# Kernel tuning notes

Hardware: AMD Instinct MI355X
Metric: run time of the kernel (lower is better)

## Reference

```python
import jax, jax.numpy as jnp
import numpy as np

N_PAIRS = 300_000
N_CENTERS = 10_000
N_SPECIES = 4
N_PSEUDO = 4
N_RADIAL = 20
L_MAX = 3


def setup_inputs() -> dict:
    key = jax.random.key(0)
    ks = jax.random.split(key, 8)
    inp = {}
    for l in range(L_MAX + 1):
        inp[f"vec_l{l}"] = jax.random.normal(ks[l], (N_PAIRS, 2 * l + 1, N_RADIAL), dtype=jnp.float32)
    # combination_matrix: Linear(n_species -> n_pseudo, bias=False) => weight [n_pseudo, n_species]
    inp["W"] = jax.random.normal(ks[4], (N_PSEUDO, N_SPECIES), dtype=jnp.float32) / np.sqrt(N_SPECIES)
    inp["species_neighbor"] = jax.random.randint(ks[5], (N_PAIRS,), 0, N_SPECIES, dtype=jnp.int64)
    inp["density_indices"] = jax.random.randint(ks[6], (N_PAIRS,), 0, N_CENTERS, dtype=jnp.int64)
    inp["n_centers"] = N_CENTERS
    return inp


def reference(vec_l0, vec_l1, vec_l2, vec_l3, W, species_neighbor, density_indices, n_centers):
    # one-hot species of neighbor, then Linear (no bias): weights [P, n_pseudo]
    one_hot_aj = jax.nn.one_hot(species_neighbor, W.shape[1], dtype=W.dtype)
    pseudo_w = one_hot_aj @ W.T  # [P, n_pseudo]
    outs = []
    for vec in (vec_l0, vec_l1, vec_l2, vec_l3):
        # outer product: [P, 2l+1, n_radial, n_pseudo]
        src = jnp.einsum('pcn,pd->pcnd', vec, pseudo_w)
        # scatter-add over unique (structure, center) groups
        dens = jax.ops.segment_sum(src, density_indices, num_segments=n_centers)
        nc, comp, nl, npse = dens.shape
        # [n_centers, 2l+1, n_pseudo, n_radial] -> flatten (pseudo-major features)
        dens = dens.swapaxes(2, 3).reshape(nc, comp * npse * nl)
        outs.append(dens)
    # concatenate all l-channels for a single output array
    return jnp.concatenate(outs, axis=1)
```

## Files before the change

### kernel.cpp

```cpp
#include <hip/hip_runtime.h>

#define N_PAIRS   300000
#define N_CENTERS 10000
#define N_FEAT    1280
#define PF        4


__global__ void hist_k(const int* __restrict__ didx, int* __restrict__ counts) {
    int p = blockIdx.x * blockDim.x + threadIdx.x;
    if (p < N_PAIRS) atomicAdd(&counts[didx[p]], 1);
}

__global__ void scan_k(const int* __restrict__ counts,
                       int* __restrict__ offsets, int* __restrict__ cursor) {
    __shared__ int part[1024];
    int t = threadIdx.x;
    const int CH = 10;
    int base = t * CH;
    int loc[CH];
    int s = 0;
    #pragma unroll
    for (int j = 0; j < CH; ++j) {
        int v = (base + j < N_CENTERS) ? counts[base + j] : 0;
        loc[j] = s; s += v;
    }
    part[t] = s;
    __syncthreads();
    for (int off = 1; off < 1024; off <<= 1) {
        int v   = part[t];
        int add = (t >= off) ? part[t - off] : 0;
        __syncthreads();
        part[t] = v + add;
        __syncthreads();
    }
    int prefix = (t > 0) ? part[t - 1] : 0;
    #pragma unroll
    for (int j = 0; j < CH; ++j) {
        int idx = base + j;
        if (idx < N_CENTERS) {
            int o = prefix + loc[j];
            offsets[idx] = o;
            cursor[idx]  = o;
        }
    }
    if (t == 1023) offsets[N_CENTERS] = part[1023];
}

__global__ void scatter_k(const int* __restrict__ didx,
                          int* __restrict__ cursor, int* __restrict__ pair_ids) {
    int p = blockIdx.x * blockDim.x + threadIdx.x;
    if (p < N_PAIRS) {
        int c = didx[p];
        int pos = atomicAdd(&cursor[c], 1);
        pair_ids[pos] = p;
    }
}


__global__ __launch_bounds__(320) void accum_k(
    const float* __restrict__ vec0, const float* __restrict__ vec1,
    const float* __restrict__ vec2, const float* __restrict__ vec3,
    const float* __restrict__ W,    const int* __restrict__ species,
    const int* __restrict__ offsets, const int* __restrict__ pair_ids,
    float* __restrict__ out) {
    __shared__ float  ldsW[16];
    __shared__ float  ldsWp[PF * 4];
    __shared__ float4 ldsv[PF * 80];

    const int t = threadIdx.x;
    const int c = blockIdx.x;
    if (t < 16) ldsW[t] = W[t];

    const int q = t / 80;
    const int u = t - q * 80;

    const float* src; int rowlen, foff;
    if (u < 5)       { src = vec0; rowlen = 20;  foff = u;      }
    else if (u < 20) { src = vec1; rowlen = 60;  foff = u - 5;  }
    else if (u < 45) { src = vec2; rowlen = 100; foff = u - 20; }
    else             { src = vec3; rowlen = 140; foff = u - 45; }

    const int g0 = 4 * u;
    int fb, vb;
    if (g0 < 20)       { fb = 0;   vb = 0;   }
    else if (g0 < 80)  { fb = 80;  vb = 20;  }
    else if (g0 < 180) { fb = 320; vb = 80;  }
    else               { fb = 720; vb = 180; }
    const int rr = g0 - vb;
    const int cc = rr / 20;
    const int n0 = rr - cc * 20;
    const int f0 = fb + cc * 80 + q * 20 + n0;

    float4 acc = make_float4(0.f, 0.f, 0.f, 0.f);
    const int start = offsets[c];
    const int end   = offsets[c + 1];
    __syncthreads();

    for (int i0 = start; i0 < end; i0 += PF) {
        const int i = i0 + q;
        if (i < end) {
            const int p = pair_ids[i];
            const float4* s4 = (const float4*)(src + (long long)p * rowlen);
            ldsv[q * 80 + u] = s4[foff];
            if (u == 0) {
                const int s = species[p];
                ldsWp[q * 4 + 0] = ldsW[0 * 4 + s];
                ldsWp[q * 4 + 1] = ldsW[1 * 4 + s];
                ldsWp[q * 4 + 2] = ldsW[2 * 4 + s];
                ldsWp[q * 4 + 3] = ldsW[3 * 4 + s];
            }
        }
        __syncthreads();
        const int nq = min(PF, end - i0);
        for (int q2 = 0; q2 < nq; ++q2) {
            const float  w = ldsWp[q2 * 4 + q];
            const float4 v = ldsv[q2 * 80 + u];
            acc.x += v.x * w; acc.y += v.y * w;
            acc.z += v.z * w; acc.w += v.w * w;
        }
        __syncthreads();
    }
    ((float4*)(out + (long long)c * N_FEAT))[f0 >> 2] = acc;
}

extern "C" void kernel_launch(void* const* d_in, const int* in_sizes, int n_in,
                              void* d_out, int out_size, void* d_ws, size_t ws_size,
                              hipStream_t stream) {
    const float* vec0 = (const float*)d_in[0];
    const float* vec1 = (const float*)d_in[1];
    const float* vec2 = (const float*)d_in[2];
    const float* vec3 = (const float*)d_in[3];
    const float* W    = (const float*)d_in[4];
    const int* species = (const int*)d_in[5];
    const int* didx    = (const int*)d_in[6];
    float* out = (float*)d_out;

    int* ws       = (int*)d_ws;
    int* counts   = ws;
    int* offsets  = ws + 16384;
    int* cursor   = ws + 32768;
    int* pair_ids = ws + 49152;

    hipMemsetAsync(counts, 0, N_CENTERS * sizeof(int), stream);
    const int nb = (N_PAIRS + 255) / 256;
    hist_k   <<<nb, 256, 0, stream>>>(didx, counts);
    scan_k   <<<1, 1024, 0, stream>>>(counts, offsets, cursor);
    scatter_k<<<nb, 256, 0, stream>>>(didx, cursor, pair_ids);
    accum_k  <<<N_CENTERS, 320, 0, stream>>>(vec0, vec1, vec2, vec3, W, species,
                                             offsets, pair_ids, out);
}
```

Measured before the change: 490.5 us.

## Remap accum threads to pseudo-channel lanes, pack species into pair ids, pad atomics

The accumulation kernel now maps each thread to a (float4 slot, pseudo channel) pair. Each thread loops over all pairs of a center directly, keeps its W row in registers, and unrolls by four. This removes the shared-memory staging and the two barriers per chunk. Species is packed into the upper bits of the sorted pair id during scatter, which removes a dependent gather, and the histogram and cursor counters are padded to cut atomic contention. As a trade-off, each float4 of input is now loaded four times, once per pseudo lane, and must be served by cache, and the packing assumes pair indices fit in 20 bits.

```diff
diff --git a/kernel.cpp b/kernel.cpp
--- a/kernel.cpp
+++ b/kernel.cpp
@@ -3,16 +3,15 @@
 #define N_PAIRS   300000
 #define N_CENTERS 10000
 #define N_FEAT    1280
-#define PF        4
 
 
-__global__ void hist_k(const int* __restrict__ didx, int* __restrict__ counts) {
+__global__ void hist_k(const int* __restrict__ didx, int* __restrict__ counts, int pad) {
     int p = blockIdx.x * blockDim.x + threadIdx.x;
-    if (p < N_PAIRS) atomicAdd(&counts[didx[p]], 1);
+    if (p < N_PAIRS) atomicAdd(&counts[didx[p] * pad], 1);
 }
 
 __global__ void scan_k(const int* __restrict__ counts,
-                       int* __restrict__ offsets, int* __restrict__ cursor) {
+                       int* __restrict__ offsets, int* __restrict__ cursor, int pad) {
     __shared__ int part[1024];
     int t = threadIdx.x;
     const int CH = 10;
@@ -21,7 +20,7 @@
     int s = 0;
     #pragma unroll
     for (int j = 0; j < CH; ++j) {
-        int v = (base + j < N_CENTERS) ? counts[base + j] : 0;
+        int v = (base + j < N_CENTERS) ? counts[(base + j) * pad] : 0;
         loc[j] = s; s += v;
     }
     part[t] = s;
@@ -40,19 +39,19 @@
         if (idx < N_CENTERS) {
             int o = prefix + loc[j];
             offsets[idx] = o;
-            cursor[idx]  = o;
+            cursor[idx * pad] = o;
         }
     }
     if (t == 1023) offsets[N_CENTERS] = part[1023];
 }
 
-__global__ void scatter_k(const int* __restrict__ didx,
-                          int* __restrict__ cursor, int* __restrict__ pair_ids) {
+__global__ void scatter_k(const int* __restrict__ didx, const int* __restrict__ species,
+                          int* __restrict__ cursor, int* __restrict__ pairs, int pad) {
     int p = blockIdx.x * blockDim.x + threadIdx.x;
     if (p < N_PAIRS) {
         int c = didx[p];
-        int pos = atomicAdd(&cursor[c], 1);
-        pair_ids[pos] = p;
+        int pos = atomicAdd(&cursor[c * pad], 1);
+        pairs[pos] = p | (species[p] << 20);
     }
 }
 
@@ -60,25 +59,19 @@
 __global__ __launch_bounds__(320) void accum_k(
     const float* __restrict__ vec0, const float* __restrict__ vec1,
     const float* __restrict__ vec2, const float* __restrict__ vec3,
-    const float* __restrict__ W,    const int* __restrict__ species,
-    const int* __restrict__ offsets, const int* __restrict__ pair_ids,
+    const float* __restrict__ W,
+    const int* __restrict__ offsets, const int* __restrict__ pairs,
     float* __restrict__ out) {
-    __shared__ float  ldsW[16];
-    __shared__ float  ldsWp[PF * 4];
-    __shared__ float4 ldsv[PF * 80];
-
     const int t = threadIdx.x;
     const int c = blockIdx.x;
-    if (t < 16) ldsW[t] = W[t];
+    const int d = t & 3;
+    const int u = t >> 2;
 
-    const int q = t / 80;
-    const int u = t - q * 80;
-
-    const float* src; int rowlen, foff;
-    if (u < 5)       { src = vec0; rowlen = 20;  foff = u;      }
-    else if (u < 20) { src = vec1; rowlen = 60;  foff = u - 5;  }
-    else if (u < 45) { src = vec2; rowlen = 100; foff = u - 20; }
-    else             { src = vec3; rowlen = 140; foff = u - 45; }
+    const float4* src4; int s4len, foff;
+    if (u < 5)       { src4 = (const float4*)vec0; s4len = 5;  foff = u;      }
+    else if (u < 20) { src4 = (const float4*)vec1; s4len = 15; foff = u - 5;  }
+    else if (u < 45) { src4 = (const float4*)vec2; s4len = 25; foff = u - 20; }
+    else             { src4 = (const float4*)vec3; s4len = 35; foff = u - 45; }
 
     const int g0 = 4 * u;
     int fb, vb;
@@ -89,37 +82,40 @@
     const int rr = g0 - vb;
     const int cc = rr / 20;
     const int n0 = rr - cc * 20;
-    const int f0 = fb + cc * 80 + q * 20 + n0;
+    const int f0 = fb + cc * 80 + d * 20 + n0;
+
+    const float w0 = W[d * 4 + 0], w1 = W[d * 4 + 1];
+    const float w2 = W[d * 4 + 2], w3 = W[d * 4 + 3];
 
     float4 acc = make_float4(0.f, 0.f, 0.f, 0.f);
-    const int start = offsets[c];
-    const int end   = offsets[c + 1];
-    __syncthreads();
+    int i = offsets[c];
+    const int end = offsets[c + 1];
 
-    for (int i0 = start; i0 < end; i0 += PF) {
-        const int i = i0 + q;
-        if (i < end) {
-            const int p = pair_ids[i];
-            const float4* s4 = (const float4*)(src + (long long)p * rowlen);
-            ldsv[q * 80 + u] = s4[foff];
-            if (u == 0) {
-                const int s = species[p];
-                ldsWp[q * 4 + 0] = ldsW[0 * 4 + s];
-                ldsWp[q * 4 + 1] = ldsW[1 * 4 + s];
-                ldsWp[q * 4 + 2] = ldsW[2 * 4 + s];
-                ldsWp[q * 4 + 3] = ldsW[3 * 4 + s];
-            }
-        }
-        __syncthreads();
-        const int nq = min(PF, end - i0);
-        for (int q2 = 0; q2 < nq; ++q2) {
-            const float  w = ldsWp[q2 * 4 + q];
-            const float4 v = ldsv[q2 * 80 + u];
-            acc.x += v.x * w; acc.y += v.y * w;
-            acc.z += v.z * w; acc.w += v.w * w;
-        }
-        __syncthreads();
+    #define LOADV(pk, v, w)                                            \
+        {   int p_ = (pk) & 0xFFFFF;                                   \
+            int s_ = (pk) >> 20;                                       \
+            v = src4[(long long)p_ * s4len + foff];                    \
+            w = (s_ == 0) ? w0 : (s_ == 1) ? w1 : (s_ == 2) ? w2 : w3; }
+
+    for (; i + 4 <= end; i += 4) {
+        const int pk0 = pairs[i], pk1 = pairs[i + 1];
+        const int pk2 = pairs[i + 2], pk3 = pairs[i + 3];
+        float4 v0, v1, v2, v3; float a0, a1, a2, a3;
+        LOADV(pk0, v0, a0); LOADV(pk1, v1, a1);
+        LOADV(pk2, v2, a2); LOADV(pk3, v3, a3);
+        acc.x += v0.x * a0; acc.y += v0.y * a0; acc.z += v0.z * a0; acc.w += v0.w * a0;
+        acc.x += v1.x * a1; acc.y += v1.y * a1; acc.z += v1.z * a1; acc.w += v1.w * a1;
+        acc.x += v2.x * a2; acc.y += v2.y * a2; acc.z += v2.z * a2; acc.w += v2.w * a2;
+        acc.x += v3.x * a3; acc.y += v3.y * a3; acc.z += v3.z * a3; acc.w += v3.w * a3;
     }
+    for (; i < end; ++i) {
+        const int pk = pairs[i];
+        float4 v; float a;
+        LOADV(pk, v, a);
+        acc.x += v.x * a; acc.y += v.y * a; acc.z += v.z * a; acc.w += v.w * a;
+    }
+    #undef LOADV
+
     ((float4*)(out + (long long)c * N_FEAT))[f0 >> 2] = acc;
 }
 
@@ -135,17 +131,22 @@
     const int* didx    = (const int*)d_in[6];
     float* out = (float*)d_out;
 
+    size_t fixed = (size_t)(N_CENTERS + 1 + N_PAIRS) * 4;
+    int pad = 1;
+    if (ws_size >= fixed + (size_t)2 * N_CENTERS * 16 * 4 + 4096) pad = 16;
+    else if (ws_size >= fixed + (size_t)2 * N_CENTERS * 4 * 4 + 4096) pad = 4;
+
     int* ws       = (int*)d_ws;
     int* counts   = ws;
-    int* offsets  = ws + 16384;
-    int* cursor   = ws + 32768;
-    int* pair_ids = ws + 49152;
+    int* cursor   = counts + (size_t)N_CENTERS * pad;
+    int* offsets  = cursor + (size_t)N_CENTERS * pad;
+    int* pairs    = offsets + (N_CENTERS + 1);
 
-    hipMemsetAsync(counts, 0, N_CENTERS * sizeof(int), stream);
+    hipMemsetAsync(counts, 0, (size_t)N_CENTERS * pad * sizeof(int), stream);
     const int nb = (N_PAIRS + 255) / 256;
-    hist_k   <<<nb, 256, 0, stream>>>(didx, counts);
-    scan_k   <<<1, 1024, 0, stream>>>(counts, offsets, cursor);
-    scatter_k<<<nb, 256, 0, stream>>>(didx, cursor, pair_ids);
-    accum_k  <<<N_CENTERS, 320, 0, stream>>>(vec0, vec1, vec2, vec3, W, species,
-                                             offsets, pair_ids, out);
+    hist_k   <<<nb, 256, 0, stream>>>(didx, counts, pad);
+    scan_k   <<<1, 1024, 0, stream>>>(counts, offsets, cursor, pad);
+    scatter_k<<<nb, 256, 0, stream>>>(didx, species, cursor, pairs, pad);
+    accum_k  <<<N_CENTERS, 320, 0, stream>>>(vec0, vec1, vec2, vec3, W,
+                                             offsets, pairs, out);
 }
```

Result: faster. 462.3 us (-5.8%).
